# Kernel optimization log

Measured on AMD Instinct MI355X. Metric: run time of the kernel, lower is better.

## Reference

```python
import jax, jax.numpy as jnp
import numpy as np

B, S, D = 16, 1024, 1024      # batch, seq_len (== max_ctx_k), input_dim (== embed_dim)
H = 1                          # num_heads (module's v-reshape requires 1)
E = 1024                       # embed_dim
TEMP = 1.0
EPS = 1e-12


def setup_inputs() -> dict:
    key = jax.random.key(0)
    ks = jax.random.split(key, 10)
    x = jax.random.normal(ks[0], (B, S, D), dtype=jnp.float32)
    mask = jax.random.randint(ks[1], (B, S, S), 0, 2, dtype=jnp.int32)
    # parameters (xavier-ish scales)
    Wqkv = jax.random.normal(ks[2], (2 * E, D), dtype=jnp.float32) * (1.0 / np.sqrt(D))
    bqkv = jax.random.normal(ks[3], (2 * E,), dtype=jnp.float32) * 0.02
    Wctx = jax.random.normal(ks[4], (2 * S, S), dtype=jnp.float32) * (1.0 / np.sqrt(S))
    bctx = jax.random.normal(ks[5], (2 * S,), dtype=jnp.float32) * 0.02
    Wf = jax.random.normal(ks[6], (1, 2), dtype=jnp.float32)
    bf = jax.random.normal(ks[7], (1,), dtype=jnp.float32) * 0.02
    Wo = jax.random.normal(ks[8], (D, 2 * D), dtype=jnp.float32) * (1.0 / np.sqrt(2 * D))
    bo = jax.random.normal(ks[9], (D,), dtype=jnp.float32) * 0.02
    return {"x": x, "mask": mask, "Wqkv": Wqkv, "bqkv": bqkv, "Wctx": Wctx,
            "bctx": bctx, "Wf": Wf, "bf": bf, "Wo": Wo, "bo": bo}


def reference(x, mask, Wqkv, bqkv, Wctx, bctx, Wf, bf, Wo, bo):
    head_dim = E // H
    # qkv projection -> (B, H, S, 2*head_dim)
    qkv = (jnp.einsum('bsd,ed->bse', x, Wqkv) + bqkv)
    qkv = qkv.reshape(B, S, H, 2 * head_dim).transpose(0, 2, 1, 3)
    q, k = jnp.split(qkv, 2, axis=-1)
    # v is just x per head (num_heads == 1)
    v = x.reshape(B, S, H, D).transpose(0, 2, 1, 3)          # (B, H, S, D)
    # self-attention scores (NOT scaled by sqrt(d_k), faithful to source)
    self_attn = jnp.einsum('bhqd,bhkd->bhqk', q, k)           # (B, H, S, S)
    # adjacency-derived context scores
    adj = jnp.einsum('bqd,bkd->bqk', x, x)[:, None]           # (B, 1, S, S)
    ctx_qk = jnp.einsum('bhqs,ts->bhqt', adj, Wctx) + bctx    # (B, 1, S, 2S)
    ctx_q, ctx_k = jnp.split(ctx_qk, 2, axis=-1)
    ctx_q = ctx_q / jnp.maximum(jnp.linalg.norm(ctx_q, axis=-1, keepdims=True), EPS)
    ctx_k = ctx_k / jnp.maximum(jnp.linalg.norm(ctx_k, axis=-1, keepdims=True), EPS)
    ctx_attn = jnp.einsum('bhqs,bhks->bhqk', ctx_q, ctx_k)    # (B, 1, S, S)
    # learned fuse of the two score maps: Linear(2 -> 1)
    attn = self_attn * Wf[0, 0] + ctx_attn * Wf[0, 1] + bf[0]
    attn = jax.nn.softmax(attn / TEMP, axis=-1)
    # post-softmax masking + L1 renorm
    m = (mask[:, None] != 0)                                  # (B, 1, S, S)
    attn = jnp.where(m, attn, 0.0)
    attn = attn / jnp.maximum(jnp.sum(jnp.abs(attn), axis=-1, keepdims=True), EPS)
    # value matmul and output projection
    values = jnp.einsum('bhqk,bhkd->bhqd', attn, v)           # (B, H, S, D)
    values = values.transpose(0, 2, 1, 3).reshape(B, S, D)
    o = jnp.einsum('bse,de->bsd', jnp.concatenate([x, values], axis=-1), Wo) + bo
    return o
```

## Files before the change

kernel.cpp:

```cpp
#include <hip/hip_runtime.h>
#include <hip/hip_bf16.h>

#define BB 16
#define SS 1024
#define DD 1024

typedef __hip_bfloat16 bf;
using s8v   = __attribute__((ext_vector_type(8))) short;
using f32x4 = __attribute__((ext_vector_type(4))) float;
using u16x4 = __attribute__((ext_vector_type(4))) unsigned short;

__device__ __forceinline__ void gload16(const bf* g, unsigned short* l)
{
    __builtin_amdgcn_global_load_lds(
        (const __attribute__((address_space(1))) void*)g,
        (__attribute__((address_space(3))) void*)l,
        16, 0, 0);
}

__device__ __forceinline__ void phase_barrier()
{
    __builtin_amdgcn_sched_barrier(0);
    __builtin_amdgcn_s_barrier();
    __builtin_amdgcn_sched_barrier(0);
}

template <int EP>
__global__ __launch_bounds__(512, 2) void gemm256(
    const bf* __restrict__ A, long sA, int lda, int kwrapA,
    const bf* __restrict__ B, long sB, int ldb,
    float* __restrict__ C, bf* __restrict__ Cb,
    bf* __restrict__ qp, bf* __restrict__ kp,
    long sC, int ldc, int K,
    const float* __restrict__ bias,
    const float* __restrict__ alpha_ptr, int alpha_idx,
    const float* __restrict__ addc_ptr,
    int accumulate)
{
    __shared__ __align__(16) unsigned short lds[65536];
    unsigned short* Asm = lds;
    unsigned short* Bsm = lds + 32768;

    const int tid = threadIdx.x;
    const int w = tid >> 6, l = tid & 63;
    const int wm = w >> 2, wn = w & 3;
    const int lm = l & 15, quad = l >> 4;
    const int bh = wn >> 1;
    const int bl0 = (wn & 1) * 64;

    const int m0 = blockIdx.y * 256, n0 = blockIdx.x * 256;
    const bf* Ab = A + (long)blockIdx.z * sA;
    const bf* Bb = B + (long)blockIdx.z * sB;

    const int srow = w * 16 + (l >> 3);
    const int scol = ((l & 7) ^ (l >> 3)) << 3;
    const long aoff0 = (long)srow * lda + scol;
    const long aoff1 = (long)(srow + 8) * lda + scol;
    const long boff0 = (long)srow * ldb + scol;
    const long boff1 = (long)(srow + 8) * ldb + scol;
    const int ldst = w * 1024;

    auto stageA = [&](int tt, int h) {
        int kk = tt << 6;
        if (kk >= kwrapA) kk -= kwrapA;
        const bf* g = Ab + (long)(m0 + h * 128) * lda + kk;
        unsigned short* d = Asm + (((tt & 1) << 1) + h) * 8192 + ldst;
        gload16(g + aoff0, d);
        gload16(g + aoff1, d + 512);
    };
    auto stageB = [&](int tt, int h) {
        const int kk = tt << 6;
        const bf* g = Bb + (long)(n0 + h * 128) * ldb + kk;
        unsigned short* d = Bsm + (((tt & 1) << 1) + h) * 8192 + ldst;
        gload16(g + boff0, d);
        gload16(g + boff1, d + 512);
    };
    auto rdA = [&](int d, int rl, int ks) -> s8v {
        const int off = rl * 64 + (((ks << 5) + (quad << 3)) ^ ((rl & 7) << 3));
        return *(const s8v*)(Asm + ((d << 1) + wm) * 8192 + off);
    };
    auto rdB = [&](int d, int bl, int ks) -> s8v {
        const int off = bl * 64 + (((ks << 5) + (quad << 3)) ^ ((bl & 7) << 3));
        return *(const s8v*)(Bsm + ((d << 1) + bh) * 8192 + off);
    };

    f32x4 acc[8][4];
#pragma unroll
    for (int i = 0; i < 8; ++i)
#pragma unroll
        for (int j = 0; j < 4; ++j)
            acc[i][j] = (f32x4){0.f, 0.f, 0.f, 0.f};

    const int NT = K >> 6;

    stageA(0, 0); stageA(0, 1); stageB(0, 0); stageB(0, 1);
    __builtin_amdgcn_sched_barrier(0);
    asm volatile("s_waitcnt vmcnt(4)" ::: "memory");
    __builtin_amdgcn_sched_barrier(0);
    stageA(1, 0); stageA(1, 1); stageB(1, 0);
    __builtin_amdgcn_sched_barrier(0);
    asm volatile("s_waitcnt vmcnt(6)" ::: "memory");
    __builtin_amdgcn_sched_barrier(0);
    phase_barrier();

    s8v a[8], b[4];
    for (int t = 0; t < NT; ++t) {
        const int d = t & 1;
#pragma unroll
        for (int mf = 0; mf < 4; ++mf) {
            a[mf * 2]     = rdA(d, mf * 16 + lm, 0);
            a[mf * 2 + 1] = rdA(d, mf * 16 + lm, 1);
        }
#pragma unroll
        for (int nf = 0; nf < 2; ++nf) {
            b[nf * 2]     = rdB(d, bl0 + nf * 16 + lm, 0);
            b[nf * 2 + 1] = rdB(d, bl0 + nf * 16 + lm, 1);
        }
        if (t + 1 < NT) stageB(t + 1, 1);
        phase_barrier();
        __builtin_amdgcn_s_setprio(1);
#pragma unroll
        for (int mf = 0; mf < 4; ++mf)
#pragma unroll
            for (int nf = 0; nf < 2; ++nf) {
                acc[mf][nf] = __builtin_amdgcn_mfma_f32_16x16x32_bf16(a[mf*2],   b[nf*2],   acc[mf][nf], 0, 0, 0);
                acc[mf][nf] = __builtin_amdgcn_mfma_f32_16x16x32_bf16(a[mf*2+1], b[nf*2+1], acc[mf][nf], 0, 0, 0);
            }
        __builtin_amdgcn_s_setprio(0);
        phase_barrier();
#pragma unroll
        for (int nf = 0; nf < 2; ++nf) {
            b[nf * 2]     = rdB(d, bl0 + (nf + 2) * 16 + lm, 0);
            b[nf * 2 + 1] = rdB(d, bl0 + (nf + 2) * 16 + lm, 1);
        }
        phase_barrier();
        __builtin_amdgcn_s_setprio(1);
#pragma unroll
        for (int mf = 0; mf < 4; ++mf)
#pragma unroll
            for (int nf = 0; nf < 2; ++nf) {
                acc[mf][nf+2] = __builtin_amdgcn_mfma_f32_16x16x32_bf16(a[mf*2],   b[nf*2],   acc[mf][nf+2], 0, 0, 0);
                acc[mf][nf+2] = __builtin_amdgcn_mfma_f32_16x16x32_bf16(a[mf*2+1], b[nf*2+1], acc[mf][nf+2], 0, 0, 0);
            }
        __builtin_amdgcn_s_setprio(0);
        phase_barrier();
#pragma unroll
        for (int mf = 0; mf < 4; ++mf) {
            a[mf * 2]     = rdA(d, 64 + mf * 16 + lm, 0);
            a[mf * 2 + 1] = rdA(d, 64 + mf * 16 + lm, 1);
        }
        if (t + 2 < NT) { stageA(t + 2, 0); stageA(t + 2, 1); }
        phase_barrier();
        __builtin_amdgcn_s_setprio(1);
#pragma unroll
        for (int mf = 0; mf < 4; ++mf)
#pragma unroll
            for (int nf = 0; nf < 2; ++nf) {
                acc[mf+4][nf+2] = __builtin_amdgcn_mfma_f32_16x16x32_bf16(a[mf*2],   b[nf*2],   acc[mf+4][nf+2], 0, 0, 0);
                acc[mf+4][nf+2] = __builtin_amdgcn_mfma_f32_16x16x32_bf16(a[mf*2+1], b[nf*2+1], acc[mf+4][nf+2], 0, 0, 0);
            }
        __builtin_amdgcn_s_setprio(0);
        phase_barrier();
#pragma unroll
        for (int nf = 0; nf < 2; ++nf) {
            b[nf * 2]     = rdB(d, bl0 + nf * 16 + lm, 0);
            b[nf * 2 + 1] = rdB(d, bl0 + nf * 16 + lm, 1);
        }
        if (t + 2 < NT) {
            stageB(t + 2, 0);
            __builtin_amdgcn_sched_barrier(0);
            asm volatile("s_waitcnt vmcnt(6)" ::: "memory");
            __builtin_amdgcn_sched_barrier(0);
        } else {
            __builtin_amdgcn_sched_barrier(0);
            asm volatile("s_waitcnt vmcnt(0)" ::: "memory");
            __builtin_amdgcn_sched_barrier(0);
        }
        phase_barrier();
        __builtin_amdgcn_s_setprio(1);
#pragma unroll
        for (int mf = 0; mf < 4; ++mf)
#pragma unroll
            for (int nf = 0; nf < 2; ++nf) {
                acc[mf+4][nf] = __builtin_amdgcn_mfma_f32_16x16x32_bf16(a[mf*2],   b[nf*2],   acc[mf+4][nf], 0, 0, 0);
                acc[mf+4][nf] = __builtin_amdgcn_mfma_f32_16x16x32_bf16(a[mf*2+1], b[nf*2+1], acc[mf+4][nf], 0, 0, 0);
            }
        __builtin_amdgcn_s_setprio(0);
        phase_barrier();
    }

    const float alpha = alpha_ptr ? alpha_ptr[alpha_idx] : 1.0f;
    const float addc  = addc_ptr ? addc_ptr[0] : 0.0f;
    float* Cp = C ? C + (long)blockIdx.z * sC : nullptr;
    bf* Cbp = (EP == 1) ? Cb + (long)blockIdx.z * sC : nullptr;
    bf* qpz = (EP == 2 || EP == 3) ? qp + (long)blockIdx.z * sC : nullptr;
    bf* kpz = (EP == 2 || EP == 3) ? kp + (long)blockIdx.z * sC : nullptr;

#pragma unroll
    for (int mf = 0; mf < 8; ++mf) {
#pragma unroll
        for (int nf = 0; nf < 4; ++nf) {
            const int cidx = n0 + wn * 64 + nf * 16 + lm;
            const float bv = bias ? bias[cidx] : 0.0f;
            const long rbase = m0 + wm * 128 + mf * 16 + quad * 4;
#pragma unroll
            for (int r = 0; r < 4; ++r) {
                const long row = rbase + r;
                if (EP == 2) {
                    float v = acc[mf][nf][r] + bv;
                    if (cidx < 1024) {
                        v *= alpha;
                        bf hi = __float2bfloat16(v);
                        bf lo = __float2bfloat16(v - __bfloat162float(hi));
                        qpz[row * 4096 + cidx] = hi;
                        qpz[row * 4096 + 1024 + cidx] = hi;
                        qpz[row * 4096 + 2048 + cidx] = lo;
                    } else {
                        const int c = cidx - 1024;
                        bf hi = __float2bfloat16(v);
                        bf lo = __float2bfloat16(v - __bfloat162float(hi));
                        kpz[row * 4096 + c] = hi;
                        kpz[row * 4096 + 1024 + c] = lo;
                        kpz[row * 4096 + 2048 + c] = hi;
                    }
                } else if (EP == 3) {
                    const float v = acc[mf][nf][r] + bv;
                    const bf h = __float2bfloat16(v);
                    if (cidx < 1024) qpz[row * 4096 + 3072 + cidx] = h;
                    else             kpz[row * 4096 + 3072 + (cidx - 1024)] = h;
                } else {
                    float v = alpha * acc[mf][nf][r] + addc + bv;
                    const long off = row * (long)ldc + cidx;
                    if (EP == 1) {
                        Cbp[off] = __float2bfloat16(v);
                    } else {
                        if (accumulate) v += Cp[off];
                        Cp[off] = v;
                    }
                }
            }
        }
    }
}

__device__ inline float blockReduceSum(float v, float* red)
{
#pragma unroll
    for (int off = 32; off > 0; off >>= 1) v += __shfl_xor(v, off, 64);
    __syncthreads();
    if ((threadIdx.x & 63) == 0) red[threadIdx.x >> 6] = v;
    __syncthreads();
    return red[0] + red[1] + red[2] + red[3];
}

__device__ inline float blockReduceMax(float v, float* red)
{
#pragma unroll
    for (int off = 32; off > 0; off >>= 1) v = fmaxf(v, __shfl_xor(v, off, 64));
    __syncthreads();
    if ((threadIdx.x & 63) == 0) red[threadIdx.x >> 6] = v;
    __syncthreads();
    return fmaxf(fmaxf(red[0], red[1]), fmaxf(red[2], red[3]));
}

__device__ inline void split_bf16(float v, bf& hi, bf& lo)
{
    hi = __float2bfloat16(v);
    lo = __float2bfloat16(v - __bfloat162float(hi));
}

__global__ __launch_bounds__(256) void prep_wqkv_kernel(
    const float* __restrict__ W, bf* __restrict__ wq3)
{
    long i = (long)blockIdx.x * 256 + threadIdx.x;
    long r = i >> 10; int c = (int)(i & 1023);
    bf hi, lo; split_bf16(W[i], hi, lo);
    wq3[r * 3072 + c] = hi;
    wq3[r * 3072 + 1024 + c] = hi;
    wq3[r * 3072 + 2048 + c] = lo;
}

__global__ __launch_bounds__(256) void conv_kernel(
    const float* __restrict__ src, bf* __restrict__ dst, int cols, int src_ld, long n)
{
    long i = (long)blockIdx.x * 256 + threadIdx.x;
    if (i >= n) return;
    long r = i / cols; int c = (int)(i % cols);
    dst[i] = __float2bfloat16(src[r * src_ld + c]);
}

__global__ __launch_bounds__(256) void conv_x_kernel(
    const float* __restrict__ x, bf* __restrict__ xhl, bf* __restrict__ xT1)
{
    __shared__ float t[32][33];
    const int b = blockIdx.z;
    const int c0 = blockIdx.x * 32, r0 = blockIdx.y * 32;
    const int tx = threadIdx.x & 31, ty = threadIdx.x >> 5;
    const float* xb = x + (long)b * SS * DD;
    bf* xhlb = xhl + (long)b * SS * 2048;
#pragma unroll
    for (int p = 0; p < 4; ++p) {
        const int r = ty + 8 * p;
        const float v = xb[(long)(r0 + r) * DD + c0 + tx];
        t[r][tx] = v;
        bf hi, lo; split_bf16(v, hi, lo);
        xhlb[(long)(r0 + r) * 2048 + c0 + tx] = hi;
        xhlb[(long)(r0 + r) * 2048 + 1024 + c0 + tx] = lo;
    }
    __syncthreads();
#pragma unroll
    for (int p = 0; p < 4; ++p) {
        const int rr = ty + 8 * p;
        xT1[(long)b * DD * SS + (long)(c0 + rr) * SS + r0 + tx] =
            __float2bfloat16(t[tx][rr]);
    }
}

__global__ __launch_bounds__(256) void l2norm_fuse_kernel(
    bf* __restrict__ q4, bf* __restrict__ k4, const float* __restrict__ Wf)
{
    __shared__ float red[4];
    const long row = blockIdx.x >> 1;
    const int half = blockIdx.x & 1;
    bf* p = (half ? k4 : q4) + row * 4096 + 3072;
    const int t = threadIdx.x;

    const u16x4 u = *reinterpret_cast<const u16x4*>(p + 4 * t);
    float v[4];
    float ss = 0.0f;
#pragma unroll
    for (int i = 0; i < 4; ++i) {
        unsigned short us = u[i];
        v[i] = __bfloat162float(*reinterpret_cast<const bf*>(&us));
        ss = fmaf(v[i], v[i], ss);
    }
    ss = blockReduceSum(ss, red);
    const float inv = 1.0f / fmaxf(sqrtf(ss), 1e-12f);
    const float scale = half ? inv : inv * Wf[1];
    u16x4 o;
#pragma unroll
    for (int i = 0; i < 4; ++i) {
        bf h = __float2bfloat16(v[i] * scale);
        o[i] = *reinterpret_cast<unsigned short*>(&h);
    }
    *reinterpret_cast<u16x4*>(p + 4 * t) = o;
}

__global__ __launch_bounds__(256) void softmax_mask_kernel(
    const float* __restrict__ attn, const int* __restrict__ mask, bf* __restrict__ attn_bf)
{
    __shared__ float red[4];
    const long row = blockIdx.x;
    const float* p = attn + row * SS;
    const int* mrow = mask + row * SS;
    bf* o = attn_bf + row * SS;
    const int t = threadIdx.x;

    float v[4];
    int mv[4];
#pragma unroll
    for (int i = 0; i < 4; ++i) { v[i] = p[t + 256 * i]; mv[i] = mrow[t + 256 * i]; }
    float mx = fmaxf(fmaxf(v[0], v[1]), fmaxf(v[2], v[3]));
    mx = blockReduceMax(mx, red);

    float e[4];
    float s = 0.0f;
#pragma unroll
    for (int i = 0; i < 4; ++i) { e[i] = expf(v[i] - mx); s += e[i]; }
    s = blockReduceSum(s, red);

    float l1 = 0.0f;
#pragma unroll
    for (int i = 0; i < 4; ++i) { e[i] = mv[i] ? e[i] / s : 0.0f; l1 += e[i]; }
    l1 = blockReduceSum(l1, red);
    const float inv = 1.0f / fmaxf(l1, 1e-12f);
#pragma unroll
    for (int i = 0; i < 4; ++i) o[t + 256 * i] = __float2bfloat16(e[i] * inv);
}

extern "C" void kernel_launch(void* const* d_in, const int* in_sizes, int n_in,
                              void* d_out, int out_size, void* d_ws, size_t ws_size,
                              hipStream_t stream)
{
    const float* x    = (const float*)d_in[0];
    const int*   mask = (const int*)d_in[1];
    const float* Wqkv = (const float*)d_in[2];
    const float* bqkv = (const float*)d_in[3];
    const float* Wctx = (const float*)d_in[4];
    const float* bctx = (const float*)d_in[5];
    const float* Wf   = (const float*)d_in[6];
    const float* bfp  = (const float*)d_in[7];
    const float* Wo   = (const float*)d_in[8];
    const float* bo   = (const float*)d_in[9];
    float* out = (float*)d_out;

    const long SD = (long)SS * DD;

    auto align_up = [](size_t v) { return (v + 255) & ~(size_t)255; };

    const size_t sz_wq3  = 2048L * 3072 * 2;
    const size_t sz_wctx = 2048L * 1024 * 2;
    const size_t sz_wob  = 1024L * 2048 * 2;
    const size_t SH = align_up(sz_wq3) + align_up(sz_wctx) + align_up(sz_wob);

    const size_t szXL = 1024L * 2048 * 2;
    const size_t szXT = 1024L * 1024 * 2;
    const size_t szQ4 = 1024L * 4096 * 2;
    const size_t szY  = 2048L * 1024 * 2;
    const size_t PB = align_up(szXL) + align_up(szXT) + 2 * align_up(szQ4) +
                      align_up(szY);

    int G = 16;
    while (G > 1 && SH + (size_t)G * PB > ws_size) G >>= 1;

    char* p = (char*)d_ws;
    auto take = [&](size_t bytes) { char* r = p; p += align_up(bytes); return r; };
    bf* Wq3   = (bf*)take(sz_wq3);
    bf* Wctx1 = (bf*)take(sz_wctx);
    bf* Wob   = (bf*)take(sz_wob);
    char* RX = take((size_t)G * szXL);
    char* RT = take((size_t)G * szXT);
    char* RQ = take((size_t)G * szQ4);
    char* RK = take((size_t)G * szQ4);
    char* RY = take((size_t)G * szY);

    bf*    xhl   = (bf*)RX;
    bf*    xT1   = (bf*)RT;
    bf*    Q4    = (bf*)RQ;
    bf*    K4    = (bf*)RK;
    bf*    Y1    = (bf*)RY;
    float* attn  = (float*)RY;
    bf*    attnb = (bf*)RQ;

    const dim3 blk(256);
    const dim3 blk5(512);
    const long sXL = 1024L * 2048;
    const long sAT = 1024L * 1024;
    const long sQ4 = 1024L * 4096;
    const long sY  = 2048L * 1024;

    prep_wqkv_kernel<<<dim3((2048L * 1024) / 256), blk, 0, stream>>>(Wqkv, Wq3);
    conv_kernel<<<dim3((2048L * 1024) / 256), blk, 0, stream>>>(Wctx, Wctx1, 1024, 1024, 2048L * 1024);
    conv_kernel<<<dim3((1024L * 2048) / 256), blk, 0, stream>>>(Wo, Wob, 2048, 2048, 1024L * 2048);

    for (int bc0 = 0; bc0 < BB; bc0 += G) {
        const float* xb = x + (long)bc0 * SD;
        const int M = G * 1024;

        conv_x_kernel<<<dim3(32, 32, G), blk, 0, stream>>>(xb, xhl, xT1);

        gemm256<2><<<dim3(2048 / 256, M / 256), blk5, 0, stream>>>(
            xhl, 0, 2048, 2048, Wq3, 0, 3072,
            nullptr, nullptr, Q4, K4, 0, 0, 3072,
            bqkv, Wf, 0, nullptr, 0);

        gemm256<1><<<dim3(1024 / 256, 2048 / 256, G), blk5, 0, stream>>>(
            Wctx1, 0, 1024, 1024, xT1, sAT, 1024,
            nullptr, Y1, nullptr, nullptr, sY, 1024, 1024,
            nullptr, nullptr, 0, nullptr, 0);

        gemm256<3><<<dim3(2048 / 256, 1024 / 256, G), blk5, 0, stream>>>(
            xhl, sXL, 2048, 1024, Y1, sY, 1024,
            nullptr, nullptr, Q4, K4, sQ4, 0, 1024,
            bctx, nullptr, 0, nullptr, 0);

        l2norm_fuse_kernel<<<dim3(G * 1024 * 2), blk, 0, stream>>>(Q4, K4, Wf);

        gemm256<0><<<dim3(1024 / 256, 1024 / 256, G), blk5, 0, stream>>>(
            Q4, sQ4, 4096, 4096, K4, sQ4, 4096,
            attn, nullptr, nullptr, nullptr, sAT, 1024, 4096,
            nullptr, nullptr, 0, bfp, 0);

        softmax_mask_kernel<<<dim3(G * 1024), blk, 0, stream>>>(
            attn, mask + (long)bc0 * SS * SS, attnb);

        gemm256<1><<<dim3(1024 / 256, 1024 / 256, G), blk5, 0, stream>>>(
            attnb, sAT, 1024, 1024, xT1, sAT, 1024,
            nullptr, xhl + 1024, nullptr, nullptr, sXL, 2048, 1024,
            nullptr, nullptr, 0, nullptr, 0);

        gemm256<0><<<dim3(1024 / 256, M / 256), blk5, 0, stream>>>(
            xhl, 0, 2048, 2048, Wob, 0, 2048,
            out + (long)bc0 * SD, nullptr, nullptr, nullptr, 0, 1024, 2048,
            bo, nullptr, 0, nullptr, 0);
    }
}
```

Measured before the change: 1.150 ms.

## Deduplicate split-bf16 Q/K/W buffers via segment-indexed K loads and remap workgroups across XCDs

```diff
diff --git a/kernel.cpp b/kernel.cpp
--- a/kernel.cpp
+++ b/kernel.cpp
@@ -18,17 +18,10 @@
         16, 0, 0);
 }
 
-__device__ __forceinline__ void phase_barrier()
-{
-    __builtin_amdgcn_sched_barrier(0);
-    __builtin_amdgcn_s_barrier();
-    __builtin_amdgcn_sched_barrier(0);
-}
-
 template <int EP>
 __global__ __launch_bounds__(512, 2) void gemm256(
-    const bf* __restrict__ A, long sA, int lda, int kwrapA,
-    const bf* __restrict__ B, long sB, int ldb,
+    const bf* __restrict__ A, long sA, int lda, int segA,
+    const bf* __restrict__ B, long sB, int ldb, int segB,
     float* __restrict__ C, bf* __restrict__ Cb,
     bf* __restrict__ qp, bf* __restrict__ kp,
     long sC, int ldc, int K,
@@ -41,6 +34,15 @@
     unsigned short* Asm = lds;
     unsigned short* Bsm = lds + 32768;
 
+    const int gx = gridDim.x, gy = gridDim.y;
+    const int nwg = gx * gy * (int)gridDim.z;
+    int lid = blockIdx.x + gx * (blockIdx.y + gy * blockIdx.z);
+    lid = (lid & 7) * (nwg >> 3) + (lid >> 3);
+    const int bx = lid % gx;
+    const int rem = lid / gx;
+    const int by = rem % gy;
+    const int bz = rem / gy;
+
     const int tid = threadIdx.x;
     const int w = tid >> 6, l = tid & 63;
     const int wm = w >> 2, wn = w & 3;
@@ -48,9 +50,9 @@
     const int bh = wn >> 1;
     const int bl0 = (wn & 1) * 64;
 
-    const int m0 = blockIdx.y * 256, n0 = blockIdx.x * 256;
-    const bf* Ab = A + (long)blockIdx.z * sA;
-    const bf* Bb = B + (long)blockIdx.z * sB;
+    const int m0 = by * 256, n0 = bx * 256;
+    const bf* Ab = A + (long)bz * sA;
+    const bf* Bb = B + (long)bz * sB;
 
     const int srow = w * 16 + (l >> 3);
     const int scol = ((l & 7) ^ (l >> 3)) << 3;
@@ -61,15 +63,16 @@
     const int ldst = w * 1024;
 
     auto stageA = [&](int tt, int h) {
-        int kk = tt << 6;
-        if (kk >= kwrapA) kk -= kwrapA;
+        const int kk = ((tt & 15) << 6) +
+                       ((((unsigned)segA >> ((tt >> 4) << 3)) & 0xffu) << 10);
         const bf* g = Ab + (long)(m0 + h * 128) * lda + kk;
         unsigned short* d = Asm + (((tt & 1) << 1) + h) * 8192 + ldst;
         gload16(g + aoff0, d);
         gload16(g + aoff1, d + 512);
     };
     auto stageB = [&](int tt, int h) {
-        const int kk = tt << 6;
+        const int kk = ((tt & 15) << 6) +
+                       ((((unsigned)segB >> ((tt >> 4) << 3)) & 0xffu) << 10);
         const bf* g = Bb + (long)(n0 + h * 128) * ldb + kk;
         unsigned short* d = Bsm + (((tt & 1) << 1) + h) * 8192 + ldst;
         gload16(g + boff0, d);
@@ -94,14 +97,10 @@
     const int NT = K >> 6;
 
     stageA(0, 0); stageA(0, 1); stageB(0, 0); stageB(0, 1);
-    __builtin_amdgcn_sched_barrier(0);
     asm volatile("s_waitcnt vmcnt(4)" ::: "memory");
-    __builtin_amdgcn_sched_barrier(0);
     stageA(1, 0); stageA(1, 1); stageB(1, 0);
-    __builtin_amdgcn_sched_barrier(0);
     asm volatile("s_waitcnt vmcnt(6)" ::: "memory");
-    __builtin_amdgcn_sched_barrier(0);
-    phase_barrier();
+    __builtin_amdgcn_s_barrier();
 
     s8v a[8], b[4];
     for (int t = 0; t < NT; ++t) {
@@ -117,7 +116,7 @@
             b[nf * 2 + 1] = rdB(d, bl0 + nf * 16 + lm, 1);
         }
         if (t + 1 < NT) stageB(t + 1, 1);
-        phase_barrier();
+        __builtin_amdgcn_s_barrier();
         __builtin_amdgcn_s_setprio(1);
 #pragma unroll
         for (int mf = 0; mf < 4; ++mf)
@@ -127,13 +126,13 @@
                 acc[mf][nf] = __builtin_amdgcn_mfma_f32_16x16x32_bf16(a[mf*2+1], b[nf*2+1], acc[mf][nf], 0, 0, 0);
             }
         __builtin_amdgcn_s_setprio(0);
-        phase_barrier();
+        __builtin_amdgcn_s_barrier();
 #pragma unroll
         for (int nf = 0; nf < 2; ++nf) {
             b[nf * 2]     = rdB(d, bl0 + (nf + 2) * 16 + lm, 0);
             b[nf * 2 + 1] = rdB(d, bl0 + (nf + 2) * 16 + lm, 1);
         }
-        phase_barrier();
+        __builtin_amdgcn_s_barrier();
         __builtin_amdgcn_s_setprio(1);
 #pragma unroll
         for (int mf = 0; mf < 4; ++mf)
@@ -143,14 +142,14 @@
                 acc[mf][nf+2] = __builtin_amdgcn_mfma_f32_16x16x32_bf16(a[mf*2+1], b[nf*2+1], acc[mf][nf+2], 0, 0, 0);
             }
         __builtin_amdgcn_s_setprio(0);
-        phase_barrier();
+        __builtin_amdgcn_s_barrier();
 #pragma unroll
         for (int mf = 0; mf < 4; ++mf) {
             a[mf * 2]     = rdA(d, 64 + mf * 16 + lm, 0);
             a[mf * 2 + 1] = rdA(d, 64 + mf * 16 + lm, 1);
         }
         if (t + 2 < NT) { stageA(t + 2, 0); stageA(t + 2, 1); }
-        phase_barrier();
+        __builtin_amdgcn_s_barrier();
         __builtin_amdgcn_s_setprio(1);
 #pragma unroll
         for (int mf = 0; mf < 4; ++mf)
@@ -160,7 +159,7 @@
                 acc[mf+4][nf+2] = __builtin_amdgcn_mfma_f32_16x16x32_bf16(a[mf*2+1], b[nf*2+1], acc[mf+4][nf+2], 0, 0, 0);
             }
         __builtin_amdgcn_s_setprio(0);
-        phase_barrier();
+        __builtin_amdgcn_s_barrier();
 #pragma unroll
         for (int nf = 0; nf < 2; ++nf) {
             b[nf * 2]     = rdB(d, bl0 + nf * 16 + lm, 0);
@@ -168,15 +167,11 @@
         }
         if (t + 2 < NT) {
             stageB(t + 2, 0);
-            __builtin_amdgcn_sched_barrier(0);
             asm volatile("s_waitcnt vmcnt(6)" ::: "memory");
-            __builtin_amdgcn_sched_barrier(0);
         } else {
-            __builtin_amdgcn_sched_barrier(0);
             asm volatile("s_waitcnt vmcnt(0)" ::: "memory");
-            __builtin_amdgcn_sched_barrier(0);
-        }
-        phase_barrier();
+        }
+        __builtin_amdgcn_s_barrier();
         __builtin_amdgcn_s_setprio(1);
 #pragma unroll
         for (int mf = 0; mf < 4; ++mf)
@@ -186,15 +181,15 @@
                 acc[mf+4][nf] = __builtin_amdgcn_mfma_f32_16x16x32_bf16(a[mf*2+1], b[nf*2+1], acc[mf+4][nf], 0, 0, 0);
             }
         __builtin_amdgcn_s_setprio(0);
-        phase_barrier();
+        __builtin_amdgcn_s_barrier();
     }
 
     const float alpha = alpha_ptr ? alpha_ptr[alpha_idx] : 1.0f;
     const float addc  = addc_ptr ? addc_ptr[0] : 0.0f;
-    float* Cp = C ? C + (long)blockIdx.z * sC : nullptr;
-    bf* Cbp = (EP == 1) ? Cb + (long)blockIdx.z * sC : nullptr;
-    bf* qpz = (EP == 2 || EP == 3) ? qp + (long)blockIdx.z * sC : nullptr;
-    bf* kpz = (EP == 2 || EP == 3) ? kp + (long)blockIdx.z * sC : nullptr;
+    float* Cp = C ? C + (long)bz * sC : nullptr;
+    bf* Cbp = (EP == 1) ? Cb + (long)bz * sC : nullptr;
+    bf* qpz = (EP == 2 || EP == 3) ? qp + (long)bz * sC : nullptr;
+    bf* kpz = (EP == 2 || EP == 3) ? kp + (long)bz * sC : nullptr;
 
 #pragma unroll
     for (int mf = 0; mf < 8; ++mf) {
@@ -212,22 +207,20 @@
                         v *= alpha;
                         bf hi = __float2bfloat16(v);
                         bf lo = __float2bfloat16(v - __bfloat162float(hi));
-                        qpz[row * 4096 + cidx] = hi;
-                        qpz[row * 4096 + 1024 + cidx] = hi;
-                        qpz[row * 4096 + 2048 + cidx] = lo;
+                        qpz[row * 3072 + cidx] = hi;
+                        qpz[row * 3072 + 1024 + cidx] = lo;
                     } else {
                         const int c = cidx - 1024;
                         bf hi = __float2bfloat16(v);
                         bf lo = __float2bfloat16(v - __bfloat162float(hi));
-                        kpz[row * 4096 + c] = hi;
-                        kpz[row * 4096 + 1024 + c] = lo;
-                        kpz[row * 4096 + 2048 + c] = hi;
+                        kpz[row * 3072 + c] = hi;
+                        kpz[row * 3072 + 1024 + c] = lo;
                     }
                 } else if (EP == 3) {
                     const float v = acc[mf][nf][r] + bv;
                     const bf h = __float2bfloat16(v);
-                    if (cidx < 1024) qpz[row * 4096 + 3072 + cidx] = h;
-                    else             kpz[row * 4096 + 3072 + (cidx - 1024)] = h;
+                    if (cidx < 1024) qpz[row * 3072 + 2048 + cidx] = h;
+                    else             kpz[row * 3072 + 2048 + (cidx - 1024)] = h;
                 } else {
                     float v = alpha * acc[mf][nf][r] + addc + bv;
                     const long off = row * (long)ldc + cidx;
@@ -270,14 +263,13 @@
 }
 
 __global__ __launch_bounds__(256) void prep_wqkv_kernel(
-    const float* __restrict__ W, bf* __restrict__ wq3)
+    const float* __restrict__ W, bf* __restrict__ wq2)
 {
     long i = (long)blockIdx.x * 256 + threadIdx.x;
     long r = i >> 10; int c = (int)(i & 1023);
     bf hi, lo; split_bf16(W[i], hi, lo);
-    wq3[r * 3072 + c] = hi;
-    wq3[r * 3072 + 1024 + c] = hi;
-    wq3[r * 3072 + 2048 + c] = lo;
+    wq2[r * 2048 + c] = hi;
+    wq2[r * 2048 + 1024 + c] = lo;
 }
 
 __global__ __launch_bounds__(256) void conv_kernel(
@@ -317,12 +309,12 @@
 }
 
 __global__ __launch_bounds__(256) void l2norm_fuse_kernel(
-    bf* __restrict__ q4, bf* __restrict__ k4, const float* __restrict__ Wf)
+    bf* __restrict__ q3, bf* __restrict__ k3, const float* __restrict__ Wf)
 {
     __shared__ float red[4];
     const long row = blockIdx.x >> 1;
     const int half = blockIdx.x & 1;
-    bf* p = (half ? k4 : q4) + row * 4096 + 3072;
+    bf* p = (half ? k3 : q3) + row * 3072 + 2048;
     const int t = threadIdx.x;
 
     const u16x4 u = *reinterpret_cast<const u16x4*>(p + 4 * t);
@@ -398,16 +390,16 @@
 
     auto align_up = [](size_t v) { return (v + 255) & ~(size_t)255; };
 
-    const size_t sz_wq3  = 2048L * 3072 * 2;
+    const size_t sz_wq2  = 2048L * 2048 * 2;
     const size_t sz_wctx = 2048L * 1024 * 2;
     const size_t sz_wob  = 1024L * 2048 * 2;
-    const size_t SH = align_up(sz_wq3) + align_up(sz_wctx) + align_up(sz_wob);
+    const size_t SH = align_up(sz_wq2) + align_up(sz_wctx) + align_up(sz_wob);
 
     const size_t szXL = 1024L * 2048 * 2;
     const size_t szXT = 1024L * 1024 * 2;
-    const size_t szQ4 = 1024L * 4096 * 2;
+    const size_t szQ3 = 1024L * 3072 * 2;
     const size_t szY  = 2048L * 1024 * 2;
-    const size_t PB = align_up(szXL) + align_up(szXT) + 2 * align_up(szQ4) +
+    const size_t PB = align_up(szXL) + align_up(szXT) + 2 * align_up(szQ3) +
                       align_up(szY);
 
     int G = 16;
@@ -415,19 +407,19 @@
 
     char* p = (char*)d_ws;
     auto take = [&](size_t bytes) { char* r = p; p += align_up(bytes); return r; };
-    bf* Wq3   = (bf*)take(sz_wq3);
+    bf* Wq2   = (bf*)take(sz_wq2);
     bf* Wctx1 = (bf*)take(sz_wctx);
     bf* Wob   = (bf*)take(sz_wob);
     char* RX = take((size_t)G * szXL);
     char* RT = take((size_t)G * szXT);
-    char* RQ = take((size_t)G * szQ4);
-    char* RK = take((size_t)G * szQ4);
+    char* RQ = take((size_t)G * szQ3);
+    char* RK = take((size_t)G * szQ3);
     char* RY = take((size_t)G * szY);
 
     bf*    xhl   = (bf*)RX;
     bf*    xT1   = (bf*)RT;
-    bf*    Q4    = (bf*)RQ;
-    bf*    K4    = (bf*)RK;
+    bf*    Q3    = (bf*)RQ;
+    bf*    K3    = (bf*)RK;
     bf*    Y1    = (bf*)RY;
     float* attn  = (float*)RY;
     bf*    attnb = (bf*)RQ;
@@ -436,10 +428,16 @@
     const dim3 blk5(512);
     const long sXL = 1024L * 2048;
     const long sAT = 1024L * 1024;
-    const long sQ4 = 1024L * 4096;
+    const long sQ3 = 1024L * 3072;
     const long sY  = 2048L * 1024;
 
-    prep_wqkv_kernel<<<dim3((2048L * 1024) / 256), blk, 0, stream>>>(Wqkv, Wq3);
+    const int segQKV_A = 0x0100;
+    const int segQKV_B = 0x010000;
+    const int segATT_A = 0x02010000;
+    const int segATT_B = 0x02000100;
+    const int segOUT   = 0x0100;
+
+    prep_wqkv_kernel<<<dim3((2048L * 1024) / 256), blk, 0, stream>>>(Wqkv, Wq2);
     conv_kernel<<<dim3((2048L * 1024) / 256), blk, 0, stream>>>(Wctx, Wctx1, 1024, 1024, 2048L * 1024);
     conv_kernel<<<dim3((1024L * 2048) / 256), blk, 0, stream>>>(Wo, Wob, 2048, 2048, 1024L * 2048);
 
@@ -450,24 +448,24 @@
         conv_x_kernel<<<dim3(32, 32, G), blk, 0, stream>>>(xb, xhl, xT1);
 
         gemm256<2><<<dim3(2048 / 256, M / 256), blk5, 0, stream>>>(
-            xhl, 0, 2048, 2048, Wq3, 0, 3072,
-            nullptr, nullptr, Q4, K4, 0, 0, 3072,
+            xhl, 0, 2048, segQKV_A, Wq2, 0, 2048, segQKV_B,
+            nullptr, nullptr, Q3, K3, 0, 0, 3072,
             bqkv, Wf, 0, nullptr, 0);
 
         gemm256<1><<<dim3(1024 / 256, 2048 / 256, G), blk5, 0, stream>>>(
-            Wctx1, 0, 1024, 1024, xT1, sAT, 1024,
+            Wctx1, 0, 1024, 0, xT1, sAT, 1024, 0,
             nullptr, Y1, nullptr, nullptr, sY, 1024, 1024,
             nullptr, nullptr, 0, nullptr, 0);
 
         gemm256<3><<<dim3(2048 / 256, 1024 / 256, G), blk5, 0, stream>>>(
-            xhl, sXL, 2048, 1024, Y1, sY, 1024,
-            nullptr, nullptr, Q4, K4, sQ4, 0, 1024,
+            xhl, sXL, 2048, 0, Y1, sY, 1024, 0,
+            nullptr, nullptr, Q3, K3, sQ3, 0, 1024,
             bctx, nullptr, 0, nullptr, 0);
 
-        l2norm_fuse_kernel<<<dim3(G * 1024 * 2), blk, 0, stream>>>(Q4, K4, Wf);
+        l2norm_fuse_kernel<<<dim3(G * 1024 * 2), blk, 0, stream>>>(Q3, K3, Wf);
 
         gemm256<0><<<dim3(1024 / 256, 1024 / 256, G), blk5, 0, stream>>>(
-            Q4, sQ4, 4096, 4096, K4, sQ4, 4096,
+            Q3, sQ3, 3072, segATT_A, K3, sQ3, 3072, segATT_B,
             attn, nullptr, nullptr, nullptr, sAT, 1024, 4096,
             nullptr, nullptr, 0, bfp, 0);
 
@@ -475,12 +473,12 @@
             attn, mask + (long)bc0 * SS * SS, attnb);
 
         gemm256<1><<<dim3(1024 / 256, 1024 / 256, G), blk5, 0, stream>>>(
-            attnb, sAT, 1024, 1024, xT1, sAT, 1024,
+            attnb, sAT, 1024, 0, xT1, sAT, 1024, 0,
             nullptr, xhl + 1024, nullptr, nullptr, sXL, 2048, 1024,
             nullptr, nullptr, 0, nullptr, 0);
 
         gemm256<0><<<dim3(1024 / 256, M / 256), blk5, 0, stream>>>(
-            xhl, 0, 2048, 2048, Wob, 0, 2048,
+            xhl, 0, 2048, segOUT, Wob, 0, 2048, segOUT,
             out + (long)bc0 * SD, nullptr, nullptr, nullptr, 0, 1024, 2048,
             bo, nullptr, 0, nullptr, 0);
     }
```

Result: faster. 1.013 ms (-12.0%).
